# Kernel optimization log

Hardware: AMD Instinct MI355X
Metric: run time of the kernel (lower is better)

## Reference

```python
import jax, jax.numpy as jnp
import numpy as np

N = 100000   # nodes
E = 300000   # edges
D = 256      # emb_dim
FD = 512     # feat_dim
L = 5        # num_layer
G = 4000     # num graphs
NUM_ATOM = 100
NUM_BOND = 2
EPS = 1e-5


def setup_inputs() -> dict:
    key = jax.random.key(0)
    ks = jax.random.split(key, 24)
    s = 0.02
    inp = {
        "atomics": jax.random.randint(ks[0], (N,), 0, NUM_ATOM, dtype=jnp.int32),
        "pos": jax.random.normal(ks[1], (N, 3), dtype=jnp.float32),
        "edge_index": jax.random.randint(ks[2], (2, E), 0, N, dtype=jnp.int32),
        "edge_attr": jax.random.randint(ks[3], (E,), 0, NUM_BOND, dtype=jnp.int32),
        "batch": jnp.sort(jax.random.randint(ks[4], (N,), 0, G, dtype=jnp.int32)),
        # parameters
        "x_emb1": jax.random.normal(ks[5], (NUM_ATOM, D)) * s,
        "x_emb2_w": jax.random.normal(ks[6], (3, D)) * s,
        "x_emb2_b": jnp.zeros((D,), jnp.float32),
        "edge_emb": jax.random.normal(ks[7], (L, NUM_BOND, D)) * s,
        "mlp_w1": jax.random.normal(ks[8], (L, D, 2 * D)) * s,
        "mlp_b1": jnp.zeros((L, 2 * D), jnp.float32),
        "mlp_w2": jax.random.normal(ks[9], (L, 2 * D, D)) * s,
        "mlp_b2": jnp.zeros((L, D), jnp.float32),
        "bn_gamma": jnp.ones((L, D), jnp.float32),
        "bn_beta": jnp.zeros((L, D), jnp.float32),
        "feat_w": jax.random.normal(ks[10], (D, FD)) * s,
        "feat_b": jnp.zeros((FD,), jnp.float32),
        "head_w1": jax.random.normal(ks[11], (FD, FD // 2)) * s,
        "head_b1": jnp.zeros((FD // 2,), jnp.float32),
        "head_w2": jax.random.normal(ks[12], (FD // 2, 1)) * s,
        "head_b2": jnp.zeros((1,), jnp.float32),
    }
    return inp


def reference(atomics, pos, edge_index, edge_attr, batch,
              x_emb1, x_emb2_w, x_emb2_b, edge_emb,
              mlp_w1, mlp_b1, mlp_w2, mlp_b2, bn_gamma, bn_beta,
              feat_w, feat_b, head_w1, head_b1, head_w2, head_b2):
    n = atomics.shape[0]
    # initial node features: atom-type embedding + linear(pos)
    h = x_emb1[atomics] + pos @ x_emb2_w + x_emb2_b
    # add self loops (self-loop bond type = NUM_BOND-1)
    loop = jnp.arange(n, dtype=edge_index.dtype)
    src = jnp.concatenate([edge_index[0], loop])           # x_j (source)
    dst = jnp.concatenate([edge_index[1], loop])           # aggregate target
    eattr = jnp.concatenate([edge_attr,
                             jnp.full((n,), NUM_BOND - 1, dtype=edge_attr.dtype)])
    for l in range(L):
        msg = h[src] + edge_emb[l][eattr]                  # [E+N, D]
        agg = jax.ops.segment_sum(msg, dst, num_segments=n)
        # GINEConv MLP: Linear -> Softplus -> Linear
        h = jax.nn.softplus(agg @ mlp_w1[l] + mlp_b1[l]) @ mlp_w2[l] + mlp_b2[l]
        # BatchNorm1d (training mode: batch statistics, biased var)
        mean = h.mean(axis=0)
        var = h.var(axis=0)
        h = (h - mean) / jnp.sqrt(var + EPS) * bn_gamma[l] + bn_beta[l]
        if l < L - 1:
            h = jax.nn.softplus(h)
        # dropout with drop_ratio=0 is a no-op
    feat = h @ feat_w + feat_b                             # [N, FD]
    # global mean pool over graphs
    ssum = jax.ops.segment_sum(feat, batch, num_segments=G)
    cnt = jax.ops.segment_sum(jnp.ones((n,), feat.dtype), batch, num_segments=G)
    gfeat = ssum / jnp.maximum(cnt, 1.0)[:, None]          # [G, FD]
    hid = jax.nn.softplus(gfeat @ head_w1 + head_b1)
    return hid @ head_w2 + head_b2                          # [G, 1]
```

## Files before the change

kernel.cpp:

```cpp
#include <hip/hip_runtime.h>
#include <hip/hip_bf16.h>
#include <hip/hip_fp16.h>
#include <stdint.h>

#define D_  256
#define FD_ 512
#define L_  5
#define EPS_ 1e-5f

#define PLANE_SH 1056
#define TILE_SH  4224

typedef unsigned short ushort_t;
typedef __attribute__((ext_vector_type(8))) _Float16 h8v;
typedef __attribute__((ext_vector_type(4))) float    f4v;

__device__ __forceinline__ float sp(float x) {
    float t = __expf(-fabsf(x));
    return fmaxf(x, 0.f) + __logf(1.f + t);
}

__device__ __forceinline__ ushort_t f2h_bits(float v) {
    union { _Float16 h; ushort_t u; } c;
    c.h = (_Float16)v;
    return c.u;
}

__device__ __forceinline__ float h2f(ushort_t u) {
    union { ushort_t u; _Float16 h; } c;
    c.u = u;
    return (float)c.h;
}

__device__ __forceinline__ uint32_t pk2(float a, float b) {
    return (uint32_t)f2h_bits(a) | ((uint32_t)f2h_bits(b) << 16);
}

__device__ __forceinline__ size_t pk_off(int gm, int gn, int nKB) {
    return ((size_t)(gm >> 7) * nKB + (gn >> 5)) * TILE_SH
         + (size_t)((gn >> 3) & 3) * PLANE_SH
         + (gm & 127) * 8 + (gn & 7);
}

__global__ __launch_bounds__(256)
void init_h_kernel(const int* __restrict__ atomics, const float* __restrict__ pos,
                   const float* __restrict__ emb1, const float* __restrict__ w2,
                   const float* __restrict__ b2, ushort_t* __restrict__ h16, int N)
{
    int i = blockIdx.x;
    int d = threadIdx.x;
    int a = atomics[i];
    float p0 = pos[(size_t)i * 3 + 0];
    float p1 = pos[(size_t)i * 3 + 1];
    float p2 = pos[(size_t)i * 3 + 2];
    float v = emb1[(size_t)a * D_ + d]
            + p0 * w2[0 * D_ + d]
            + p1 * w2[1 * D_ + d]
            + p2 * w2[2 * D_ + d]
            + b2[d];
    h16[(size_t)i * D_ + d] = f2h_bits(v);
}

__global__ __launch_bounds__(256)
void hist_kernel(const int* __restrict__ dst, int* __restrict__ cnt, int E)
{
    int e = blockIdx.x * 256 + threadIdx.x;
    if (e < E) atomicAdd(&cnt[dst[e]], 1);
}

__global__ __launch_bounds__(256)
void alloc_kernel(const int* __restrict__ cnt, int* __restrict__ start,
                  int* __restrict__ cursor, int* __restrict__ total, int N)
{
    int i = blockIdx.x * 256 + threadIdx.x;
    if (i < N) {
        int s = atomicAdd(total, cnt[i]);
        start[i] = s;
        cursor[i] = s;
    }
}

__global__ __launch_bounds__(256)
void fill_kernel(const int* __restrict__ src, const int* __restrict__ dst,
                 const int* __restrict__ attr, int* __restrict__ cursor,
                 uint32_t* __restrict__ elist, int E)
{
    int e = blockIdx.x * 256 + threadIdx.x;
    if (e < E) {
        int p = atomicAdd(&cursor[dst[e]], 1);
        elist[p] = (uint32_t)src[e] | ((uint32_t)attr[e] << 30);
    }
}

__global__ __launch_bounds__(256)
void range_kernel(const int* __restrict__ batch, int* __restrict__ gstart,
                  int* __restrict__ gend, int N)
{
    int i = blockIdx.x * 256 + threadIdx.x;
    if (i >= N) return;
    int b = batch[i];
    if (i == 0 || batch[i - 1] != b) gstart[b] = i;
    if (i == N - 1 || batch[i + 1] != b) gend[b] = i + 1;
}

template <int DOACT>
__global__ __launch_bounds__(256)
void gather_act8_kernel(const ushort_t* __restrict__ h16, const uint32_t* __restrict__ elist,
                        const int* __restrict__ start, const int* __restrict__ cnt,
                        const float* __restrict__ ee_l,
                        const float* __restrict__ bnsum, const float* __restrict__ gamma,
                        const float* __restrict__ beta, float invN,
                        ushort_t* __restrict__ aggP, int N)
{
    int i0 = blockIdx.x * 8;
    int d = threadIdx.x;
    float sc = 1.f, sh = 0.f;
    if (DOACT) {
        float mean = bnsum[d] * invN;
        float var = bnsum[D_ + d] * invN - mean * mean;
        sc = gamma[d] * rsqrtf(fmaxf(var, 0.f) + EPS_);
        sh = beta[d] - mean * sc;
    }
    float ee0 = ee_l[d];
    float ee1 = ee_l[D_ + d];
    int base[8], deg[8];
    float a[8];
    int mdeg = 0;
#pragma unroll
    for (int r = 0; r < 8; ++r) {
        int i = i0 + r;
        base[r] = 0; deg[r] = 0; a[r] = 0.f;
        if (i < N) {
            base[r] = start[i];
            deg[r] = cnt[i];
            float v = h2f(h16[(size_t)i * D_ + d]);
            if (DOACT) v = sp(v * sc + sh);
            a[r] = v + ee1;
            mdeg = (deg[r] > mdeg) ? deg[r] : mdeg;
        }
    }
    for (int j = 0; j < mdeg; ++j) {
        uint32_t p[8];
#pragma unroll
        for (int r = 0; r < 8; ++r) {
            int idx = (j < deg[r]) ? (base[r] + j) : 0;
            p[r] = elist[idx];
        }
        float v[8];
#pragma unroll
        for (int r = 0; r < 8; ++r) {
            int s = p[r] & 0x3FFFFFFF;
            float t = h2f(h16[(size_t)s * D_ + d]);
            if (DOACT) t = sp(t * sc + sh);
            v[r] = t + ((p[r] >> 30) ? ee1 : ee0);
        }
#pragma unroll
        for (int r = 0; r < 8; ++r)
            if (j < deg[r]) a[r] += v[r];
    }
#pragma unroll
    for (int r = 0; r < 8; ++r) {
        int i = i0 + r;
        if (i < N) aggP[pk_off(i, d, 8)] = f2h_bits(a[r]);
    }
}

__global__ __launch_bounds__(256)
void pool_bn_kernel(const ushort_t* __restrict__ h16, const float* __restrict__ bnsum,
                    const float* __restrict__ gamma, const float* __restrict__ beta,
                    const int* __restrict__ gstart, const int* __restrict__ gend,
                    ushort_t* __restrict__ poolP, float invN)
{
    int g = blockIdx.x;
    int d = threadIdx.x;
    float mean = bnsum[d] * invN;
    float var = bnsum[D_ + d] * invN - mean * mean;
    float sc = gamma[d] * rsqrtf(fmaxf(var, 0.f) + EPS_);
    float sh = beta[d] - mean * sc;
    int s0 = gstart[g], s1 = gend[g];
    float acc = 0.f;
    int i = s0;
    for (; i + 4 <= s1; i += 4) {
        float a0 = h2f(h16[(size_t)(i + 0) * D_ + d]);
        float a1 = h2f(h16[(size_t)(i + 1) * D_ + d]);
        float a2 = h2f(h16[(size_t)(i + 2) * D_ + d]);
        float a3 = h2f(h16[(size_t)(i + 3) * D_ + d]);
        acc += (a0 + a1) + (a2 + a3);
    }
    for (; i < s1; ++i)
        acc += h2f(h16[(size_t)i * D_ + d]);
    int cnt = s1 - s0;
    float mval = (cnt > 0) ? (sc * acc / (float)cnt + sh) : 0.f;
    poolP[pk_off(g, d, 8)] = f2h_bits(mval);
}

__global__ __launch_bounds__(256)
void convert_w_pack(const float* __restrict__ W, ushort_t* __restrict__ dh,
                    int N, int nKB)
{
    int kb = blockIdx.x, nb = blockIdx.y;
    int n = threadIdx.x >> 1, half = threadIdx.x & 1;
#pragma unroll
    for (int j = 0; j < 2; ++j) {
        int kq = half * 2 + j;
        size_t o = (size_t)(nb * nKB + kb) * TILE_SH + kq * PLANE_SH + n * 8;
#pragma unroll
        for (int jj = 0; jj < 8; ++jj) {
            float w = W[(size_t)(kb * 32 + kq * 8 + jj) * N + nb * 128 + n];
            dh[o + jj] = f2h_bits(w);
        }
    }
}

__global__ __launch_bounds__(512, 4)
void fused_mlp_kernel(const ushort_t* __restrict__ APK,
                      const ushort_t* __restrict__ W1P,
                      const ushort_t* __restrict__ W2P,
                      const float* __restrict__ b1,
                      const float* __restrict__ b2,
                      ushort_t* __restrict__ Hout,
                      float* __restrict__ bnsum,
                      int m)
{
    __shared__ ushort_t Tl[32768];

    int rb = blockIdx.x;
    int tid = threadIdx.x, w = tid >> 6, lane = tid & 63;
    int fr = lane & 15, kq = lane >> 4;

    const ushort_t* aT = APK + (size_t)(rb >> 1) * (8 * TILE_SH)
                       + (size_t)kq * PLANE_SH + (size_t)((rb & 1) * 64 + fr) * 8;
    const ushort_t* bT = W1P + (size_t)(w >> 1) * (8 * TILE_SH)
                       + (size_t)kq * PLANE_SH + (size_t)((w & 1) * 64 + fr) * 8;

    f4v acc1[4][4];
#pragma unroll
    for (int i = 0; i < 4; ++i)
#pragma unroll
        for (int j = 0; j < 4; ++j)
            acc1[i][j] = (f4v){0.f, 0.f, 0.f, 0.f};

    for (int kb = 0; kb < 8; ++kb) {
        h8v Af[4], Wf[4];
#pragma unroll
        for (int t = 0; t < 4; ++t) {
            Af[t] = *(const h8v*)(aT + (size_t)kb * TILE_SH + t * 128);
            Wf[t] = *(const h8v*)(bT + (size_t)kb * TILE_SH + t * 128);
        }
        __builtin_amdgcn_s_setprio(1);
#pragma unroll
        for (int nt = 0; nt < 4; ++nt)
#pragma unroll
            for (int mt = 0; mt < 4; ++mt)
                acc1[nt][mt] = __builtin_amdgcn_mfma_f32_16x16x32_f16(
                    Wf[nt], Af[mt], acc1[nt][mt], 0, 0, 0);
        __builtin_amdgcn_s_setprio(0);
    }

#pragma unroll
    for (int nt = 0; nt < 4; ++nt) {
        float4 b1v = *(const float4*)(b1 + w * 64 + nt * 16 + kq * 4);
        int baseu = (w * 2 + (nt >> 1)) * 2048
                  + ((nt & 1) * 2 + (kq >> 1)) * 512
                  + (kq & 1) * 4;
#pragma unroll
        for (int mt = 0; mt < 4; ++mt) {
            uint2 val;
            val.x = pk2(sp(acc1[nt][mt][0] + b1v.x), sp(acc1[nt][mt][1] + b1v.y));
            val.y = pk2(sp(acc1[nt][mt][2] + b1v.z), sp(acc1[nt][mt][3] + b1v.w));
            *(uint2*)(Tl + baseu + (mt * 16 + fr) * 8) = val;
        }
    }
    __syncthreads();

    const ushort_t* wT = W2P + (size_t)(w >> 2) * (16 * TILE_SH)
                       + (size_t)kq * PLANE_SH + (size_t)((w & 3) * 32 + fr) * 8;

    f4v acc2[4][2];
#pragma unroll
    for (int i = 0; i < 4; ++i)
#pragma unroll
        for (int j = 0; j < 2; ++j)
            acc2[i][j] = (f4v){0.f, 0.f, 0.f, 0.f};

    for (int kb = 0; kb < 16; ++kb) {
        h8v Tf[4], Wf[2];
#pragma unroll
        for (int t = 0; t < 4; ++t)
            Tf[t] = *(const h8v*)(Tl + kb * 2048 + kq * 512 + (fr + t * 16) * 8);
#pragma unroll
        for (int t = 0; t < 2; ++t)
            Wf[t] = *(const h8v*)(wT + (size_t)kb * TILE_SH + t * 128);
        __builtin_amdgcn_s_setprio(1);
#pragma unroll
        for (int rt = 0; rt < 4; ++rt)
#pragma unroll
            for (int ct = 0; ct < 2; ++ct)
                acc2[rt][ct] = __builtin_amdgcn_mfma_f32_16x16x32_f16(
                    Tf[rt], Wf[ct], acc2[rt][ct], 0, 0, 0);
        __builtin_amdgcn_s_setprio(0);
    }

    int gm0 = rb * 64 + kq * 4;
#pragma unroll
    for (int ct = 0; ct < 2; ++ct) {
        int gn = w * 32 + ct * 16 + fr;
        float bv = b2[gn];
        float s = 0.f, ss = 0.f;
#pragma unroll
        for (int rt = 0; rt < 4; ++rt)
#pragma unroll
            for (int rr = 0; rr < 4; ++rr) {
                int gm = gm0 + rt * 16 + rr;
                if (gm < m) {
                    float v = acc2[rt][ct][rr] + bv;
                    Hout[(size_t)gm * D_ + gn] = f2h_bits(v);
                    s += v;
                    ss += v * v;
                }
            }
        s  += __shfl_xor(s, 16);  s  += __shfl_xor(s, 32);
        ss += __shfl_xor(ss, 16); ss += __shfl_xor(ss, 32);
        if (kq == 0) {
            atomicAdd(&bnsum[gn], s);
            atomicAdd(&bnsum[D_ + gn], ss);
        }
    }
}

template <int EPI>
__global__ __launch_bounds__(256, 3)
void gemm_p16(const ushort_t* __restrict__ APK, const ushort_t* __restrict__ BPK,
              const float* __restrict__ bias,
              ushort_t* __restrict__ Tout, float* __restrict__ Cout,
              float* __restrict__ bnsum, const int* __restrict__ batch,
              int m, int N, int nKB)
{
    const int NB = N >> 7;
    const int mb = (m + 127) >> 7;
    int id = blockIdx.x;
    int grp = id / (8 * NB);
    int rem = id - grp * 8 * NB;
    int nb = rem >> 3;
    int rb = grp * 8 + (rem & 7);
    if (rb >= mb) return;

    int tid = threadIdx.x, wave = tid >> 6, lane = tid & 63;
    int wr = wave >> 1, wc = wave & 1;
    int fr = lane & 15, kq = lane >> 4;

    const ushort_t* aP = APK + (size_t)rb * nKB * TILE_SH
                       + (size_t)kq * PLANE_SH + (size_t)(wr * 64 + fr) * 8;
    const ushort_t* bP = BPK + (size_t)nb * nKB * TILE_SH
                       + (size_t)kq * PLANE_SH + (size_t)(wc * 64 + fr) * 8;

    f4v acc[4][4];
#pragma unroll
    for (int i = 0; i < 4; ++i)
#pragma unroll
        for (int j = 0; j < 4; ++j)
            acc[i][j] = (f4v){0.f, 0.f, 0.f, 0.f};

    h8v Fa[4], Fb[4], Ga[4], Gb[4];

#define LOADF(dA, dB, kbi)                                                   \
    {   const ushort_t* ap_ = aP + (size_t)(kbi) * TILE_SH;                  \
        const ushort_t* bp_ = bP + (size_t)(kbi) * TILE_SH;                  \
        _Pragma("unroll")                                                    \
        for (int t = 0; t < 4; ++t) {                                        \
            dA[t] = *(const h8v*)(ap_ + t * 128);                            \
            dB[t] = *(const h8v*)(bp_ + t * 128);                            \
        } }

#define MFMA16(sA, sB)                                                       \
    {   __builtin_amdgcn_s_setprio(1);                                       \
        _Pragma("unroll")                                                    \
        for (int rt = 0; rt < 4; ++rt)                                       \
            _Pragma("unroll")                                                \
            for (int ct = 0; ct < 4; ++ct)                                   \
                acc[rt][ct] = __builtin_amdgcn_mfma_f32_16x16x32_f16(        \
                    sA[rt], sB[ct], acc[rt][ct], 0, 0, 0);                   \
        __builtin_amdgcn_s_setprio(0); }

    LOADF(Fa, Fb, 0);
    for (int kb = 0; kb < nKB; kb += 2) {
        LOADF(Ga, Gb, kb + 1);
        MFMA16(Fa, Fb);
        if (kb + 2 < nKB) LOADF(Fa, Fb, kb + 2);
        MFMA16(Ga, Gb);
    }
#undef LOADF
#undef MFMA16

    int gm00 = rb * 128 + wr * 64 + kq * 4;
    int gn0  = nb * 128 + wc * 64 + fr;
    int nKBo = N >> 5;
    size_t tileRow = (size_t)(rb * nKBo + nb * 4 + wc * 2) * TILE_SH
                   + (size_t)((wr * 64 + kq * 4) * 8 + (fr & 7));
#pragma unroll
    for (int ct = 0; ct < 4; ++ct) {
        int gn = gn0 + ct * 16;
        float bv = bias[gn];
        float s = 0.f, ss = 0.f;
        size_t cb = tileRow + (size_t)(ct >> 1) * TILE_SH
                  + (size_t)((2 * ct + (fr >> 3)) & 3) * PLANE_SH;
#pragma unroll
        for (int rt = 0; rt < 4; ++rt) {
            if (EPI == 2) {
                int bp = -1; float run = 0.f;
#pragma unroll
                for (int rr = 0; rr < 4; ++rr) {
                    int gm = gm00 + rt * 16 + rr;
                    if (gm >= m) continue;
                    float v = acc[rt][ct][rr] + bv;
                    int bg = batch[gm];
                    if (bg == bp) { run += v; }
                    else {
                        if (bp >= 0) atomicAdd(&Cout[(size_t)bp * N + gn], run);
                        bp = bg; run = v;
                    }
                }
                if (bp >= 0) atomicAdd(&Cout[(size_t)bp * N + gn], run);
            } else {
#pragma unroll
                for (int rr = 0; rr < 4; ++rr) {
                    int gm = gm00 + rt * 16 + rr;
                    if (gm >= m) continue;
                    float v = acc[rt][ct][rr] + bv;
                    if (EPI == 0) {
                        Tout[cb + (rt * 16 + rr) * 8] = f2h_bits(sp(v));
                    } else if (EPI == 1) {
                        Tout[(size_t)gm * N + gn] = f2h_bits(v);
                        s += v;
                        ss += v * v;
                    } else {
                        Cout[(size_t)gm * N + gn] = v;
                    }
                }
            }
        }
        if (EPI == 1) {
            s  += __shfl_xor(s, 16);  s  += __shfl_xor(s, 32);
            ss += __shfl_xor(ss, 16); ss += __shfl_xor(ss, 32);
            if (kq == 0) {
                atomicAdd(&bnsum[gn], s);
                atomicAdd(&bnsum[D_ + gn], ss);
            }
        }
    }
}

#define BM 64
#define BN 64
#define BK 16

__global__ __launch_bounds__(256)
void gemm_head(const float* __restrict__ A, const float* __restrict__ W,
               const float* __restrict__ bias, float* __restrict__ C,
               int M, int N, int K)
{
    __shared__ float As[BK][BM + 4];
    __shared__ float Ws[BK][BN + 4];

    int tid = threadIdx.x;
    int bm = blockIdx.y * BM;
    int bn = blockIdx.x * BN;
    int tx = tid & 15;
    int ty = tid >> 4;

    float acc[4][4] = {};

    int a_m = tid >> 2;
    int a_k = (tid & 3) * 4;
    int w_k = tid >> 4;
    int w_n = (tid & 15) * 4;

    for (int k0 = 0; k0 < K; k0 += BK) {
        int gm = bm + a_m;
        float4 av = make_float4(0.f, 0.f, 0.f, 0.f);
        if (gm < M)
            av = *(const float4*)(A + (size_t)gm * K + k0 + a_k);
        As[a_k + 0][a_m] = av.x;
        As[a_k + 1][a_m] = av.y;
        As[a_k + 2][a_m] = av.z;
        As[a_k + 3][a_m] = av.w;

        float4 wv = *(const float4*)(W + (size_t)(k0 + w_k) * N + bn + w_n);
        *(float4*)&Ws[w_k][w_n] = wv;

        __syncthreads();

#pragma unroll
        for (int k = 0; k < BK; ++k) {
            float4 a4 = *(const float4*)&As[k][ty * 4];
            float4 b4 = *(const float4*)&Ws[k][tx * 4];
            float a[4] = {a4.x, a4.y, a4.z, a4.w};
            float b[4] = {b4.x, b4.y, b4.z, b4.w};
#pragma unroll
            for (int i = 0; i < 4; ++i)
#pragma unroll
                for (int j = 0; j < 4; ++j)
                    acc[i][j] += a[i] * b[j];
        }
        __syncthreads();
    }

#pragma unroll
    for (int i = 0; i < 4; ++i) {
        int gm = bm + ty * 4 + i;
        if (gm >= M) continue;
#pragma unroll
        for (int j = 0; j < 4; ++j) {
            int gn = bn + tx * 4 + j;
            C[(size_t)gm * N + gn] = sp(acc[i][j] + bias[gn]);
        }
    }
}

__global__ __launch_bounds__(256)
void head2_kernel(const float* __restrict__ hid, const float* __restrict__ w2,
                  const float* __restrict__ b2, float* __restrict__ out, int G)
{
    __shared__ float red[256];
    int g = blockIdx.x;
    int t = threadIdx.x;
    float v = hid[(size_t)g * 256 + t] * w2[t];
    red[t] = v;
    __syncthreads();
    for (int s = 128; s > 0; s >>= 1) {
        if (t < s) red[t] += red[t + s];
        __syncthreads();
    }
    if (t == 0) out[g] = red[0] + b2[0];
}

extern "C" void kernel_launch(void* const* d_in, const int* in_sizes, int n_in,
                              void* d_out, int out_size, void* d_ws, size_t ws_size,
                              hipStream_t stream)
{
    const int N = in_sizes[0];
    const int E = in_sizes[3];
    const int G = out_size;

    const int*   atomics  = (const int*)d_in[0];
    const float* pos      = (const float*)d_in[1];
    const int*   eidx     = (const int*)d_in[2];
    const int*   eattr    = (const int*)d_in[3];
    const int*   batch    = (const int*)d_in[4];
    const float* x_emb1   = (const float*)d_in[5];
    const float* x_emb2_w = (const float*)d_in[6];
    const float* x_emb2_b = (const float*)d_in[7];
    const float* edge_emb = (const float*)d_in[8];
    const float* mlp_w1   = (const float*)d_in[9];
    const float* mlp_b1   = (const float*)d_in[10];
    const float* mlp_w2   = (const float*)d_in[11];
    const float* mlp_b2   = (const float*)d_in[12];
    const float* bn_g     = (const float*)d_in[13];
    const float* bn_b     = (const float*)d_in[14];
    const float* feat_w   = (const float*)d_in[15];
    const float* feat_b   = (const float*)d_in[16];
    const float* head_w1  = (const float*)d_in[17];
    const float* head_b1  = (const float*)d_in[18];
    const float* head_w2  = (const float*)d_in[19];
    const float* head_b2  = (const float*)d_in[20];
    float* out = (float*)d_out;

    const int* src = eidx;
    const int* dst = eidx + E;

    char* ws = (char*)d_ws;
    size_t off = 0;
    auto carve = [&](size_t bytes) {
        void* p = ws + off;
        off += (bytes + 255) & ~(size_t)255;
        return p;
    };

    const int nRB = (N + 127) / 128;
    const int nGB = (G + 127) / 128;

    ushort_t* h16  = (ushort_t*)carve((size_t)N * D_ * 2);
    ushort_t* aggP = (ushort_t*)carve((size_t)nRB * 8 * TILE_SH * 2);
    const size_t WTILES = 32 * TILE_SH;
    ushort_t* w1P = (ushort_t*)carve((size_t)L_ * WTILES * 2);
    ushort_t* w2P = (ushort_t*)carve((size_t)L_ * WTILES * 2);
    ushort_t* fP  = (ushort_t*)carve(WTILES * 2);
    float* bnsum  = (float*)carve(2 * D_ * 4);
    float* gfeat  = (float*)carve((size_t)G * FD_ * 4);
    float* hid    = (float*)carve((size_t)G * (FD_ / 2) * 4);
    ushort_t* poolP = (ushort_t*)carve((size_t)nGB * 8 * TILE_SH * 2);
    int* gstart  = (int*)carve((size_t)G * 4);
    int* gend    = (int*)carve((size_t)G * 4);
    int* cnt_i   = (int*)carve((size_t)N * 4);
    int* start_i = (int*)carve((size_t)N * 4);
    int* cursor  = (int*)carve((size_t)N * 4);
    int* total   = (int*)carve(4);
    uint32_t* elist = (uint32_t*)carve((size_t)E * 4);

    const float invN = 1.f / (float)N;

    hipMemsetAsync(cnt_i, 0, (size_t)N * 4, stream);
    hipMemsetAsync(total, 0, 4, stream);
    hipMemsetAsync(gstart, 0, (size_t)G * 4, stream);
    hipMemsetAsync(gend, 0, (size_t)G * 4, stream);
    hist_kernel<<<(E + 255) / 256, 256, 0, stream>>>(dst, cnt_i, E);
    alloc_kernel<<<(N + 255) / 256, 256, 0, stream>>>(cnt_i, start_i, cursor, total, N);
    fill_kernel<<<(E + 255) / 256, 256, 0, stream>>>(src, dst, eattr, cursor, elist, E);
    range_kernel<<<(N + 255) / 256, 256, 0, stream>>>(batch, gstart, gend, N);

    for (int l = 0; l < L_; ++l) {
        convert_w_pack<<<dim3(8, 4), 256, 0, stream>>>(
            mlp_w1 + (size_t)l * D_ * FD_, w1P + (size_t)l * WTILES, FD_, 8);
        convert_w_pack<<<dim3(16, 2), 256, 0, stream>>>(
            mlp_w2 + (size_t)l * FD_ * D_, w2P + (size_t)l * WTILES, D_, 16);
    }
    convert_w_pack<<<dim3(8, 4), 256, 0, stream>>>(feat_w, fP, FD_, 8);

    init_h_kernel<<<N, 256, 0, stream>>>(atomics, pos, x_emb1, x_emb2_w, x_emb2_b, h16, N);

    const int GB8 = (N + 7) / 8;
    const int FB  = (N + 63) / 64;

    for (int l = 0; l < L_; ++l) {
        const float* ee_l = edge_emb + (size_t)l * 2 * D_;
        if (l == 0) {
            gather_act8_kernel<0><<<GB8, 256, 0, stream>>>(
                h16, elist, start_i, cnt_i, ee_l,
                bnsum, bn_g, bn_b, invN, aggP, N);
        } else {
            gather_act8_kernel<1><<<GB8, 256, 0, stream>>>(
                h16, elist, start_i, cnt_i, ee_l,
                bnsum, bn_g + (size_t)(l - 1) * D_, bn_b + (size_t)(l - 1) * D_,
                invN, aggP, N);
        }

        hipMemsetAsync(bnsum, 0, 2 * D_ * 4, stream);
        fused_mlp_kernel<<<FB, 512, 0, stream>>>(
            aggP, w1P + (size_t)l * WTILES, w2P + (size_t)l * WTILES,
            mlp_b1 + (size_t)l * FD_, mlp_b2 + (size_t)l * D_,
            h16, bnsum, N);
    }

    pool_bn_kernel<<<G, 256, 0, stream>>>(h16, bnsum, bn_g + (size_t)(L_ - 1) * D_,
                                          bn_b + (size_t)(L_ - 1) * D_,
                                          gstart, gend, poolP, invN);
    auto swgrid = [](int mb, int NBc) { return ((mb + 7) / 8) * 8 * NBc; };
    gemm_p16<3><<<swgrid(nGB, 4), 256, 0, stream>>>(
        poolP, fP, feat_b, nullptr, gfeat, nullptr, nullptr, G, FD_, 8);

    gemm_head<<<dim3((FD_ / 2) / BN, (G + BM - 1) / BM), 256, 0, stream>>>(
        gfeat, head_w1, head_b1, hid, G, FD_ / 2, FD_);
    head2_kernel<<<G, 256, 0, stream>>>(hid, head_w2, head_b2, out, G);
}
```

Baseline: 1.310 ms.

## Precompute BN+softplus activation once per node and gather with half2 loads

```diff
diff --git a/kernel.cpp b/kernel.cpp
--- a/kernel.cpp
+++ b/kernel.cpp
@@ -103,65 +103,92 @@
     if (i == N - 1 || batch[i + 1] != b) gend[b] = i + 1;
 }
 
-template <int DOACT>
-__global__ __launch_bounds__(256)
-void gather_act8_kernel(const ushort_t* __restrict__ h16, const uint32_t* __restrict__ elist,
-                        const int* __restrict__ start, const int* __restrict__ cnt,
-                        const float* __restrict__ ee_l,
-                        const float* __restrict__ bnsum, const float* __restrict__ gamma,
-                        const float* __restrict__ beta, float invN,
-                        ushort_t* __restrict__ aggP, int N)
-{
-    int i0 = blockIdx.x * 8;
-    int d = threadIdx.x;
-    float sc = 1.f, sh = 0.f;
-    if (DOACT) {
-        float mean = bnsum[d] * invN;
-        float var = bnsum[D_ + d] * invN - mean * mean;
-        sc = gamma[d] * rsqrtf(fmaxf(var, 0.f) + EPS_);
-        sh = beta[d] - mean * sc;
-    }
-    float ee0 = ee_l[d];
-    float ee1 = ee_l[D_ + d];
-    int base[8], deg[8];
-    float a[8];
+__global__ __launch_bounds__(256)
+void act16_kernel(const ushort_t* __restrict__ h16, ushort_t* __restrict__ hact,
+                  const float* __restrict__ bnsum, const float* __restrict__ gamma,
+                  const float* __restrict__ beta, long long total16, float invN)
+{
+    __shared__ float ssc[256], ssh[256];
+    int t = threadIdx.x;
+    {
+        float mean = bnsum[t] * invN;
+        float var = bnsum[D_ + t] * invN - mean * mean;
+        float sc = gamma[t] * rsqrtf(fmaxf(var, 0.f) + EPS_);
+        ssc[t] = sc;
+        ssh[t] = beta[t] - mean * sc;
+    }
+    __syncthreads();
+    long long idx = (long long)blockIdx.x * 256 + t;
+    if (idx >= total16) return;
+    int c0 = (int)((idx * 16) & 255);
+    uint4 in0 = *(const uint4*)(h16 + idx * 16);
+    uint4 in1 = *(const uint4*)(h16 + idx * 16 + 8);
+    ushort_t* ip0 = (ushort_t*)&in0;
+    ushort_t* ip1 = (ushort_t*)&in1;
+    ushort_t ov[16];
+#pragma unroll
+    for (int j = 0; j < 8; ++j)
+        ov[j] = f2h_bits(sp(h2f(ip0[j]) * ssc[c0 + j] + ssh[c0 + j]));
+#pragma unroll
+    for (int j = 0; j < 8; ++j)
+        ov[8 + j] = f2h_bits(sp(h2f(ip1[j]) * ssc[c0 + 8 + j] + ssh[c0 + 8 + j]));
+    *(uint4*)(hact + idx * 16)     = *(uint4*)&ov[0];
+    *(uint4*)(hact + idx * 16 + 8) = *(uint4*)&ov[8];
+}
+
+__global__ __launch_bounds__(256)
+void gather2_kernel(const ushort_t* __restrict__ hact, const uint32_t* __restrict__ elist,
+                    const int* __restrict__ start, const int* __restrict__ cnt,
+                    const float* __restrict__ ee_l, ushort_t* __restrict__ aggP, int N)
+{
+    int t = threadIdx.x;
+    int d0 = (t & 127) * 2;
+    int ib = blockIdx.x * 8 + (t >> 7) * 4;
+    float2 e0 = *(const float2*)(ee_l + d0);
+    float2 e1 = *(const float2*)(ee_l + D_ + d0);
+    int base[4], deg[4];
+    float ax[4], ay[4];
     int mdeg = 0;
 #pragma unroll
-    for (int r = 0; r < 8; ++r) {
-        int i = i0 + r;
-        base[r] = 0; deg[r] = 0; a[r] = 0.f;
+    for (int r = 0; r < 4; ++r) {
+        int i = ib + r;
+        base[r] = 0; deg[r] = 0; ax[r] = 0.f; ay[r] = 0.f;
         if (i < N) {
             base[r] = start[i];
             deg[r] = cnt[i];
-            float v = h2f(h16[(size_t)i * D_ + d]);
-            if (DOACT) v = sp(v * sc + sh);
-            a[r] = v + ee1;
+            uint32_t hv = *(const uint32_t*)(hact + (size_t)i * D_ + d0);
+            ax[r] = h2f((ushort_t)hv) + e1.x;
+            ay[r] = h2f((ushort_t)(hv >> 16)) + e1.y;
             mdeg = (deg[r] > mdeg) ? deg[r] : mdeg;
         }
     }
     for (int j = 0; j < mdeg; ++j) {
-        uint32_t p[8];
-#pragma unroll
-        for (int r = 0; r < 8; ++r) {
+        uint32_t p[4];
+#pragma unroll
+        for (int r = 0; r < 4; ++r) {
             int idx = (j < deg[r]) ? (base[r] + j) : 0;
             p[r] = elist[idx];
         }
-        float v[8];
-#pragma unroll
-        for (int r = 0; r < 8; ++r) {
+        float vx[4], vy[4];
+#pragma unroll
+        for (int r = 0; r < 4; ++r) {
             int s = p[r] & 0x3FFFFFFF;
-            float t = h2f(h16[(size_t)s * D_ + d]);
-            if (DOACT) t = sp(t * sc + sh);
-            v[r] = t + ((p[r] >> 30) ? ee1 : ee0);
-        }
-#pragma unroll
-        for (int r = 0; r < 8; ++r)
-            if (j < deg[r]) a[r] += v[r];
-    }
-#pragma unroll
-    for (int r = 0; r < 8; ++r) {
-        int i = i0 + r;
-        if (i < N) aggP[pk_off(i, d, 8)] = f2h_bits(a[r]);
+            uint32_t hv = *(const uint32_t*)(hact + (size_t)s * D_ + d0);
+            bool b1 = (p[r] >> 30) != 0;
+            vx[r] = h2f((ushort_t)hv) + (b1 ? e1.x : e0.x);
+            vy[r] = h2f((ushort_t)(hv >> 16)) + (b1 ? e1.y : e0.y);
+        }
+#pragma unroll
+        for (int r = 0; r < 4; ++r)
+            if (j < deg[r]) { ax[r] += vx[r]; ay[r] += vy[r]; }
+    }
+#pragma unroll
+    for (int r = 0; r < 4; ++r) {
+        int i = ib + r;
+        if (i < N) {
+            size_t o = pk_off(i, d0, 8);
+            *(uint32_t*)(aggP + o) = pk2(ax[r], ay[r]);
+        }
     }
 }
 
@@ -580,6 +607,7 @@
     const int nGB = (G + 127) / 128;
 
     ushort_t* h16  = (ushort_t*)carve((size_t)N * D_ * 2);
+    ushort_t* hact = (ushort_t*)carve((size_t)N * D_ * 2);
     ushort_t* aggP = (ushort_t*)carve((size_t)nRB * 8 * TILE_SH * 2);
     const size_t WTILES = 32 * TILE_SH;
     ushort_t* w1P = (ushort_t*)carve((size_t)L_ * WTILES * 2);
@@ -618,21 +646,22 @@
 
     init_h_kernel<<<N, 256, 0, stream>>>(atomics, pos, x_emb1, x_emb2_w, x_emb2_b, h16, N);
 
+    const long long total16 = (long long)N * D_ / 16;
+    const int ACTB = (int)((total16 + 255) / 256);
     const int GB8 = (N + 7) / 8;
     const int FB  = (N + 63) / 64;
 
     for (int l = 0; l < L_; ++l) {
         const float* ee_l = edge_emb + (size_t)l * 2 * D_;
-        if (l == 0) {
-            gather_act8_kernel<0><<<GB8, 256, 0, stream>>>(
-                h16, elist, start_i, cnt_i, ee_l,
-                bnsum, bn_g, bn_b, invN, aggP, N);
-        } else {
-            gather_act8_kernel<1><<<GB8, 256, 0, stream>>>(
-                h16, elist, start_i, cnt_i, ee_l,
-                bnsum, bn_g + (size_t)(l - 1) * D_, bn_b + (size_t)(l - 1) * D_,
-                invN, aggP, N);
-        }
+        const ushort_t* gsrc = h16;
+        if (l > 0) {
+            act16_kernel<<<ACTB, 256, 0, stream>>>(h16, hact, bnsum,
+                bn_g + (size_t)(l - 1) * D_, bn_b + (size_t)(l - 1) * D_,
+                total16, invN);
+            gsrc = hact;
+        }
+        gather2_kernel<<<GB8, 256, 0, stream>>>(gsrc, elist, start_i, cnt_i,
+                                                ee_l, aggP, N);
 
         hipMemsetAsync(bnsum, 0, 2 * D_ * 4, stream);
         fused_mlp_kernel<<<FB, 512, 0, stream>>>(
```

After: 1.153 ms. -12.0%, faster.
